# Kernel optimization log

Measured on AMD Instinct MI355X. Metric: run time of the kernel, lower is better.

Reference implementation:

```python
import jax, jax.numpy as jnp
import numpy as np

H = 8  # heads
EPS = 1e-5


def adaln(x, t, W, b):
    # AdaLayerNorm: emb = Linear(t); scale, shift = chunk(emb, 2, dim=-1)
    emb = t @ W + b                      # [B,1,2*D]
    scale, shift = jnp.split(emb, 2, axis=-1)
    mu = jnp.mean(x, axis=-1, keepdims=True)
    var = jnp.var(x, axis=-1, keepdims=True)
    xn = (x - mu) / jnp.sqrt(var + EPS)  # elementwise_affine=False
    return xn * (1.0 + scale) + shift


def attention(x, ctx, Wq, Wk, Wv, Wo, bo):
    B, N, D = x.shape
    d = D // H
    q = (x @ Wq).reshape(B, N, H, d).transpose(0, 2, 1, 3)          # [B,H,N,d]
    k = (ctx @ Wk).reshape(B, ctx.shape[1], H, d).transpose(0, 2, 1, 3)
    v = (ctx @ Wv).reshape(B, ctx.shape[1], H, d).transpose(0, 2, 1, 3)
    sim = jnp.einsum('bhid,bhjd->bhij', q, k) * (d ** -0.5)
    attn = jax.nn.softmax(sim, axis=-1)
    out = jnp.einsum('bhij,bhjd->bhid', attn, v)
    out = out.transpose(0, 2, 1, 3).reshape(B, N, D)
    return out @ Wo + bo


def geglu_ff(x, W1, b1, W2, b2):
    u, g = jnp.split(x @ W1 + b1, 2, axis=-1)
    return (u * jax.nn.gelu(g, approximate=False)) @ W2 + b2


def setup_inputs() -> dict:
    key = jax.random.key(0)
    ks = jax.random.split(key, 16)
    D = 512
    s = 0.02
    inp = {
        'x': jax.random.normal(ks[0], (2, 2048, D), jnp.float32),
        't': jax.random.normal(ks[1], (2, 1, D), jnp.float32),
        'cond': jax.random.normal(ks[2], (2, 1024, D), jnp.float32),
        'n1_w': jax.random.normal(ks[3], (D, 2 * D), jnp.float32) * s,
        'n1_b': jnp.zeros((2 * D,), jnp.float32),
        'n2_w': jax.random.normal(ks[4], (D, 2 * D), jnp.float32) * s,
        'n2_b': jnp.zeros((2 * D,), jnp.float32),
        'n4_w': jax.random.normal(ks[5], (D, 2 * D), jnp.float32) * s,
        'n4_b': jnp.zeros((2 * D,), jnp.float32),
        'a1_q': jax.random.normal(ks[6], (D, D), jnp.float32) * s,
        'a1_k': jax.random.normal(ks[7], (D, D), jnp.float32) * s,
        'a1_v': jax.random.normal(ks[8], (D, D), jnp.float32) * s,
        'a1_o': jax.random.normal(ks[9], (D, D), jnp.float32) * s,
        'a1_ob': jnp.zeros((D,), jnp.float32),
        'a2_q': jax.random.normal(ks[10], (D, D), jnp.float32) * s,
        'a2_k': jax.random.normal(ks[11], (D, D), jnp.float32) * s,
        'a2_v': jax.random.normal(ks[12], (D, D), jnp.float32) * s,
        'a2_o': jax.random.normal(ks[13], (D, D), jnp.float32) * s,
        'a2_ob': jnp.zeros((D,), jnp.float32),
        'ff_w1': jax.random.normal(ks[14], (D, 8 * D), jnp.float32) * s,
        'ff_b1': jnp.zeros((8 * D,), jnp.float32),
        'ff_w2': jax.random.normal(ks[15], (4 * D, D), jnp.float32) * s,
        'ff_b2': jnp.zeros((D,), jnp.float32),
    }
    return inp


def reference(x, t, cond, n1_w, n1_b, n2_w, n2_b, n4_w, n4_b,
              a1_q, a1_k, a1_v, a1_o, a1_ob,
              a2_q, a2_k, a2_v, a2_o, a2_ob,
              ff_w1, ff_b1, ff_w2, ff_b2):
    # BasicTransformerBlock, is_deform=False, withT=False, inference (dropout/droppath = identity, LayerScale = identity since init_values=0)
    h = adaln(x, t, n1_w, n1_b)
    x = attention(h, h, a1_q, a1_k, a1_v, a1_o, a1_ob) + x
    h = adaln(x, t, n2_w, n2_b)
    x = attention(h, cond, a2_q, a2_k, a2_v, a2_o, a2_ob) + x
    h = adaln(x, t, n4_w, n4_b)
    x = geglu_ff(h, ff_w1, ff_b1, ff_w2, ff_b2) + x
    return x
```

## Files before the change

kernel.cpp:

```cpp
#include <hip/hip_runtime.h>
#include <math.h>

#define D_MODEL 512
#define NHEADS  8
#define DHEAD   64

typedef __bf16  bf16x2 __attribute__((ext_vector_type(2)));
typedef __bf16  bf16x4 __attribute__((ext_vector_type(4)));
typedef __bf16  bf16x8 __attribute__((ext_vector_type(8)));
typedef float   f32x4  __attribute__((ext_vector_type(4)));

__global__ __launch_bounds__(256) void adaln_params_kernel(
        const float* __restrict__ t,
        const float* __restrict__ w1, const float* __restrict__ b1,
        const float* __restrict__ w2, const float* __restrict__ b2,
        const float* __restrict__ w4, const float* __restrict__ b4,
        float* __restrict__ emb, int B) {
    int g = blockIdx.x * blockDim.x + threadIdx.x;
    int per = B * 2 * D_MODEL;
    if (g >= 3 * per) return;
    int norm = g / per;
    int rem  = g - norm * per;
    int b = rem / (2 * D_MODEL);
    int c = rem % (2 * D_MODEL);
    const float* W  = (norm == 0) ? w1 : (norm == 1 ? w2 : w4);
    const float* bb = (norm == 0) ? b1 : (norm == 1 ? b2 : b4);
    const float* trow = t + (size_t)b * D_MODEL;
    float acc = bb[c];
    for (int k = 0; k < D_MODEL; ++k)
        acc = fmaf(trow[k], W[(size_t)k * (2 * D_MODEL) + c], acc);
    emb[g] = acc;
}

__global__ __launch_bounds__(256) void adaln_apply_kernel(
        const float* __restrict__ x, const float* __restrict__ emb_n,
        __bf16* __restrict__ h, int N) {
    int row = blockIdx.x;
    int b = row / N;
    const float* xr = x + (size_t)row * D_MODEL;
    int tid = threadIdx.x;
    float2 v = *(const float2*)(xr + 2 * tid);
    float s = v.x + v.y, sq = v.x * v.x + v.y * v.y;
#pragma unroll
    for (int off = 32; off; off >>= 1) {
        s  += __shfl_xor(s, off);
        sq += __shfl_xor(sq, off);
    }
    __shared__ float rs[4], rq[4];
    if ((tid & 63) == 0) { rs[tid >> 6] = s; rq[tid >> 6] = sq; }
    __syncthreads();
    float tot  = rs[0] + rs[1] + rs[2] + rs[3];
    float totq = rq[0] + rq[1] + rq[2] + rq[3];
    float mu  = tot * (1.0f / D_MODEL);
    float var = totq * (1.0f / D_MODEL) - mu * mu;
    float inv = rsqrtf(var + 1e-5f);
    const float* er = emb_n + (size_t)b * (2 * D_MODEL);
    float2 sc = *(const float2*)(er + 2 * tid);
    float2 sh = *(const float2*)(er + D_MODEL + 2 * tid);
    bf16x2 o;
    o[0] = (__bf16)((v.x - mu) * inv * (1.0f + sc.x) + sh.x);
    o[1] = (__bf16)((v.y - mu) * inv * (1.0f + sc.y) + sh.y);
    *(bf16x2*)(h + (size_t)row * D_MODEL + 2 * tid) = o;
}

__global__ __launch_bounds__(256) void convert_bf16v_kernel(
        const float* __restrict__ src, __bf16* __restrict__ dst, int n) {
    int i = (blockIdx.x * 256 + threadIdx.x) * 4;
    if (i >= n) return;
    float4 v = *(const float4*)(src + i);
    bf16x2 a, b;
    a[0] = (__bf16)v.x; a[1] = (__bf16)v.y;
    b[0] = (__bf16)v.z; b[1] = (__bf16)v.w;
    *(bf16x2*)(dst + i)     = a;
    *(bf16x2*)(dst + i + 2) = b;
}

__device__ __forceinline__ void transpose_tile(
        const float* __restrict__ src, __bf16* __restrict__ dst,
        int K, int N, int k0, int n0) {
    __shared__ float t[64][65];
    int tid = threadIdx.x;
    int r = tid >> 6, c = tid & 63;
#pragma unroll
    for (int i = 0; i < 16; ++i)
        t[r + 4 * i][c] = src[(size_t)(k0 + r + 4 * i) * N + n0 + c];
    __syncthreads();
#pragma unroll
    for (int i = 0; i < 16; ++i)
        dst[(size_t)(n0 + r + 4 * i) * K + k0 + c] = (__bf16)t[c][r + 4 * i];
}

struct WPtrs8 { const float* s[8]; __bf16* d[8]; };

__global__ __launch_bounds__(256) void convt8_kernel(WPtrs8 p) {
    int w = blockIdx.z;
    transpose_tile(p.s[w], p.d[w], 512, 512, blockIdx.y * 64, blockIdx.x * 64);
}

__global__ __launch_bounds__(256) void convt_kernel(
        const float* __restrict__ src, __bf16* __restrict__ dst, int K, int N) {
    transpose_tile(src, dst, K, N, blockIdx.y * 64, blockIdx.x * 64);
}

template<int OUT>
__global__ __launch_bounds__(256) void gemm_bf16_kernel(
        const __bf16* __restrict__ A, const __bf16* __restrict__ Bt,
        const float* __restrict__ bias, const float* __restrict__ res,
        void* __restrict__ Cv, int M, int K, int N) {
    __shared__ __attribute__((aligned(16))) __bf16 As[128][72];
    __shared__ __attribute__((aligned(16))) __bf16 Bs[64][72];
    int tid = threadIdx.x;
    int wave = tid >> 6, lane = tid & 63;
    int wr = wave >> 1, wc = wave & 1;
    int r = lane & 15, g = lane >> 4;
    int m0 = blockIdx.y << 7, n0 = blockIdx.x << 6;

    int sr = tid >> 3, sk = (tid & 7) << 3;
    const __bf16* Ap = A  + (size_t)(m0 + sr) * K + sk;
    const __bf16* Bp = Bt + (size_t)(n0 + sr) * K + sk;

    f32x4 acc[4][2];
#pragma unroll
    for (int mi = 0; mi < 4; ++mi)
#pragma unroll
        for (int ni = 0; ni < 2; ++ni) acc[mi][ni] = (f32x4){0.f, 0.f, 0.f, 0.f};

    for (int k0 = 0; k0 < K; k0 += 64) {
#pragma unroll
        for (int i = 0; i < 4; ++i)
            *(bf16x8*)&As[sr + 32 * i][sk] = *(const bf16x8*)(Ap + (size_t)(32 * i) * K + k0);
#pragma unroll
        for (int i = 0; i < 2; ++i)
            *(bf16x8*)&Bs[sr + 32 * i][sk] = *(const bf16x8*)(Bp + (size_t)(32 * i) * K + k0);
        __syncthreads();
#pragma unroll
        for (int kk = 0; kk < 2; ++kk) {
            bf16x8 af[4], bfr[2];
#pragma unroll
            for (int mi = 0; mi < 4; ++mi)
                af[mi] = *(const bf16x8*)&As[(wr << 6) + (mi << 4) + r][(kk << 5) + (g << 3)];
#pragma unroll
            for (int ni = 0; ni < 2; ++ni)
                bfr[ni] = *(const bf16x8*)&Bs[(wc << 5) + (ni << 4) + r][(kk << 5) + (g << 3)];
#pragma unroll
            for (int mi = 0; mi < 4; ++mi)
#pragma unroll
                for (int ni = 0; ni < 2; ++ni)
                    acc[mi][ni] = __builtin_amdgcn_mfma_f32_16x16x32_bf16(
                        af[mi], bfr[ni], acc[mi][ni], 0, 0, 0);
        }
        __syncthreads();
    }

#pragma unroll
    for (int mi = 0; mi < 4; ++mi) {
#pragma unroll
        for (int ni = 0; ni < 2; ++ni) {
            int col = n0 + (wc << 5) + (ni << 4) + r;
            float scl = (OUT == 2 && col < 512) ? 0.125f : 1.0f;
#pragma unroll
            for (int rg = 0; rg < 4; ++rg) {
                int row = m0 + (wr << 6) + (mi << 4) + (g << 2) + rg;
                if (OUT == 1) {
                    float v = acc[mi][ni][rg] + bias[col] + res[(size_t)row * N + col];
                    ((float*)Cv)[(size_t)row * N + col] = v;
                } else {
                    ((__bf16*)Cv)[(size_t)row * N + col] = (__bf16)(acc[mi][ni][rg] * scl);
                }
            }
        }
    }
}

__global__ __launch_bounds__(256) void gemm_geglu_bf16_kernel(
        const __bf16* __restrict__ A, const __bf16* __restrict__ W1t,
        const float* __restrict__ b1, __bf16* __restrict__ gg, int M, int K) {
    const int NOUT = 4 * D_MODEL;
    __shared__ __attribute__((aligned(16))) __bf16 As[128][72];
    __shared__ __attribute__((aligned(16))) __bf16 Bu[64][72];
    __shared__ __attribute__((aligned(16))) __bf16 Bg[64][72];
    int tid = threadIdx.x;
    int wave = tid >> 6, lane = tid & 63;
    int wr = wave >> 1, wc = wave & 1;
    int r = lane & 15, g = lane >> 4;
    int m0 = blockIdx.y << 7, n0 = blockIdx.x << 6;

    int sr = tid >> 3, sk = (tid & 7) << 3;
    const __bf16* Ap = A   + (size_t)(m0 + sr) * K + sk;
    const __bf16* Up = W1t + (size_t)(n0 + sr) * K + sk;
    const __bf16* Gp = W1t + (size_t)(NOUT + n0 + sr) * K + sk;

    f32x4 accu[4][2], accg[4][2];
#pragma unroll
    for (int mi = 0; mi < 4; ++mi)
#pragma unroll
        for (int ni = 0; ni < 2; ++ni) {
            accu[mi][ni] = (f32x4){0.f, 0.f, 0.f, 0.f};
            accg[mi][ni] = (f32x4){0.f, 0.f, 0.f, 0.f};
        }

    for (int k0 = 0; k0 < K; k0 += 64) {
#pragma unroll
        for (int i = 0; i < 4; ++i)
            *(bf16x8*)&As[sr + 32 * i][sk] = *(const bf16x8*)(Ap + (size_t)(32 * i) * K + k0);
#pragma unroll
        for (int i = 0; i < 2; ++i) {
            *(bf16x8*)&Bu[sr + 32 * i][sk] = *(const bf16x8*)(Up + (size_t)(32 * i) * K + k0);
            *(bf16x8*)&Bg[sr + 32 * i][sk] = *(const bf16x8*)(Gp + (size_t)(32 * i) * K + k0);
        }
        __syncthreads();
#pragma unroll
        for (int kk = 0; kk < 2; ++kk) {
            bf16x8 af[4], bu[2], bg[2];
#pragma unroll
            for (int mi = 0; mi < 4; ++mi)
                af[mi] = *(const bf16x8*)&As[(wr << 6) + (mi << 4) + r][(kk << 5) + (g << 3)];
#pragma unroll
            for (int ni = 0; ni < 2; ++ni) {
                bu[ni] = *(const bf16x8*)&Bu[(wc << 5) + (ni << 4) + r][(kk << 5) + (g << 3)];
                bg[ni] = *(const bf16x8*)&Bg[(wc << 5) + (ni << 4) + r][(kk << 5) + (g << 3)];
            }
#pragma unroll
            for (int mi = 0; mi < 4; ++mi)
#pragma unroll
                for (int ni = 0; ni < 2; ++ni) {
                    accu[mi][ni] = __builtin_amdgcn_mfma_f32_16x16x32_bf16(
                        af[mi], bu[ni], accu[mi][ni], 0, 0, 0);
                    accg[mi][ni] = __builtin_amdgcn_mfma_f32_16x16x32_bf16(
                        af[mi], bg[ni], accg[mi][ni], 0, 0, 0);
                }
        }
        __syncthreads();
    }

#pragma unroll
    for (int mi = 0; mi < 4; ++mi) {
#pragma unroll
        for (int ni = 0; ni < 2; ++ni) {
            int col = n0 + (wc << 5) + (ni << 4) + r;
            float bu_ = b1[col], bg_ = b1[NOUT + col];
#pragma unroll
            for (int rg = 0; rg < 4; ++rg) {
                int row = m0 + (wr << 6) + (mi << 4) + (g << 2) + rg;
                float u  = accu[mi][ni][rg] + bu_;
                float gv = accg[mi][ni][rg] + bg_;
                float ge = 0.5f * gv * (1.0f + erff(gv * 0.70710678118654752f));
                gg[(size_t)row * NOUT + col] = (__bf16)(u * ge);
            }
        }
    }
}

__global__ __launch_bounds__(256) void attn_mfma_kernel(
        const __bf16* __restrict__ q, const __bf16* __restrict__ k,
        const __bf16* __restrict__ v, __bf16* __restrict__ o,
        int Nq, int Nk, int sq, int skv) {
    __shared__ __attribute__((aligned(16))) __bf16 Ks[64][72];
    __shared__ __attribute__((aligned(16))) __bf16 Vt[64 * 72];
    __shared__ __attribute__((aligned(16))) __bf16 Pl[4][16][72];

    int tid = threadIdx.x;
    int w = tid >> 6, lane = tid & 63;
    int r = lane & 15, g = lane >> 4;

    int nqb = Nq >> 6;
    int qb = blockIdx.x % nqb;
    int hh = (blockIdx.x / nqb) % NHEADS;
    int b  = blockIdx.x / (nqb * NHEADS);

    const __bf16* qp = q + ((size_t)(b * Nq + (qb << 6) + (w << 4) + r)) * sq
                         + hh * DHEAD + (g << 3);
    bf16x8 qf0 = *(const bf16x8*)qp;
    bf16x8 qf1 = *(const bf16x8*)(qp + 32);

    int krow = tid >> 2, kcb = (tid & 3) << 4;
    int va = tid & 31,  vbb = tid >> 5;
    size_t kvbase = (size_t)b * Nk * skv + (size_t)hh * DHEAD;
    const __bf16* kp = k + kvbase + (size_t)krow * skv + kcb;
    const __bf16* vp = v + kvbase + (size_t)(2 * va) * skv + (vbb << 3);

    f32x4 oacc[4];
#pragma unroll
    for (int dt = 0; dt < 4; ++dt) oacc[dt] = (f32x4){0.f, 0.f, 0.f, 0.f};
    float m = -1e30f, l = 0.f;

    bf16x8 kr0 = *(const bf16x8*)kp;
    bf16x8 kr1 = *(const bf16x8*)(kp + 8);
    bf16x8 vr0 = *(const bf16x8*)vp;
    bf16x8 vr1 = *(const bf16x8*)(vp + skv);
    {
        *(bf16x8*)&Ks[krow][kcb]     = kr0;
        *(bf16x8*)&Ks[krow][kcb + 8] = kr1;
        int blk = (va >> 2) ^ vbb;
        int cw  = ((va & 3) << 1);
#pragma unroll
        for (int j = 0; j < 8; ++j) {
            bf16x2 pr; pr[0] = vr0[j]; pr[1] = vr1[j];
            *(bf16x2*)&Vt[(size_t)(8 * vbb + j) * 72 + blk * 8 + cw] = pr;
        }
    }
    __syncthreads();

    int ntiles = Nk >> 6;
    for (int t = 0; t < ntiles; ++t) {
        bool pre = (t + 1 < ntiles);
        if (pre) {
            const __bf16* kp2 = kp + (size_t)(t + 1) * 64 * skv;
            const __bf16* vp2 = vp + (size_t)(t + 1) * 64 * skv;
            kr0 = *(const bf16x8*)kp2;
            kr1 = *(const bf16x8*)(kp2 + 8);
            vr0 = *(const bf16x8*)vp2;
            vr1 = *(const bf16x8*)(vp2 + skv);
        }

        f32x4 sacc[4];
#pragma unroll
        for (int nt = 0; nt < 4; ++nt) sacc[nt] = (f32x4){0.f, 0.f, 0.f, 0.f};
        __builtin_amdgcn_s_setprio(1);
#pragma unroll
        for (int nt = 0; nt < 4; ++nt) {
            bf16x8 kf0 = *(const bf16x8*)&Ks[(nt << 4) + r][g << 3];
            bf16x8 kf1 = *(const bf16x8*)&Ks[(nt << 4) + r][32 + (g << 3)];
            sacc[nt] = __builtin_amdgcn_mfma_f32_16x16x32_bf16(kf0, qf0, sacc[nt], 0, 0, 0);
            sacc[nt] = __builtin_amdgcn_mfma_f32_16x16x32_bf16(kf1, qf1, sacc[nt], 0, 0, 0);
        }
        __builtin_amdgcn_s_setprio(0);

        float mx = sacc[0][0];
#pragma unroll
        for (int nt = 0; nt < 4; ++nt)
#pragma unroll
            for (int rg = 0; rg < 4; ++rg) mx = fmaxf(mx, sacc[nt][rg]);
        mx = fmaxf(mx, __shfl_xor(mx, 16));
        mx = fmaxf(mx, __shfl_xor(mx, 32));
        float mn = fmaxf(m, mx);
        float al = __expf(m - mn);
        m = mn;
        float sum = 0.f;
#pragma unroll
        for (int nt = 0; nt < 4; ++nt) {
            bf16x4 pk;
#pragma unroll
            for (int rg = 0; rg < 4; ++rg) {
                float p = __expf(sacc[nt][rg] - mn);
                sum += p;
                pk[rg] = (__bf16)p;
            }
            *(bf16x4*)&Pl[w][r][(nt << 4) + (g << 2)] = pk;
        }
        sum += __shfl_xor(sum, 16);
        sum += __shfl_xor(sum, 32);
        l = l * al + sum;
#pragma unroll
        for (int dt = 0; dt < 4; ++dt)
#pragma unroll
            for (int rg = 0; rg < 4; ++rg) oacc[dt][rg] *= al;

        __builtin_amdgcn_s_setprio(1);
#pragma unroll
        for (int kh = 0; kh < 2; ++kh) {
            bf16x8 pa = *(const bf16x8*)&Pl[w][r][(kh << 5) + (g << 3)];
#pragma unroll
            for (int dt = 0; dt < 4; ++dt) {
                int row = (dt << 4) + r;
                int blk = ((kh << 2) + g) ^ ((row >> 3) & 7);
                bf16x8 vf = *(const bf16x8*)&Vt[(size_t)row * 72 + (blk << 3)];
                oacc[dt] = __builtin_amdgcn_mfma_f32_16x16x32_bf16(vf, pa, oacc[dt], 0, 0, 0);
            }
        }
        __builtin_amdgcn_s_setprio(0);

        __syncthreads();
        if (pre) {
            *(bf16x8*)&Ks[krow][kcb]     = kr0;
            *(bf16x8*)&Ks[krow][kcb + 8] = kr1;
            int blk = (va >> 2) ^ vbb;
            int cw  = ((va & 3) << 1);
#pragma unroll
            for (int j = 0; j < 8; ++j) {
                bf16x2 pr; pr[0] = vr0[j]; pr[1] = vr1[j];
                *(bf16x2*)&Vt[(size_t)(8 * vbb + j) * 72 + blk * 8 + cw] = pr;
            }
        }
        __syncthreads();
    }

    float inv = 1.0f / l;
    __bf16* ob = o + ((size_t)(b * Nq + (qb << 6) + (w << 4) + r)) * D_MODEL + hh * DHEAD;
#pragma unroll
    for (int dt = 0; dt < 4; ++dt) {
        bf16x4 ov;
#pragma unroll
        for (int rg = 0; rg < 4; ++rg) ov[rg] = (__bf16)(oacc[dt][rg] * inv);
        *(bf16x4*)&ob[(dt << 4) + (g << 2)] = ov;
    }
}

extern "C" void kernel_launch(void* const* d_in, const int* in_sizes, int n_in,
                              void* d_out, int out_size, void* d_ws, size_t ws_size,
                              hipStream_t stream) {
    const float* x    = (const float*)d_in[0];
    const float* t    = (const float*)d_in[1];
    const float* cond = (const float*)d_in[2];
    const float* n1_w = (const float*)d_in[3];
    const float* n1_b = (const float*)d_in[4];
    const float* n2_w = (const float*)d_in[5];
    const float* n2_b = (const float*)d_in[6];
    const float* n4_w = (const float*)d_in[7];
    const float* n4_b = (const float*)d_in[8];
    const float* a1_q = (const float*)d_in[9];
    const float* a1_k = (const float*)d_in[10];
    const float* a1_v = (const float*)d_in[11];
    const float* a1_o = (const float*)d_in[12];
    const float* a1_ob= (const float*)d_in[13];
    const float* a2_q = (const float*)d_in[14];
    const float* a2_k = (const float*)d_in[15];
    const float* a2_v = (const float*)d_in[16];
    const float* a2_o = (const float*)d_in[17];
    const float* a2_ob= (const float*)d_in[18];
    const float* ff_w1= (const float*)d_in[19];
    const float* ff_b1= (const float*)d_in[20];
    const float* ff_w2= (const float*)d_in[21];
    const float* ff_b2= (const float*)d_in[22];
    float* out = (float*)d_out;

    const int B  = in_sizes[1] / D_MODEL;
    const int N  = in_sizes[0] / (B * D_MODEL);
    const int Nc = in_sizes[2] / (B * D_MODEL);
    const int R  = B * N;
    const int Rc = B * Nc;

    char* Wb = (char*)d_ws;
    float* emb   = (float*)Wb;
    __bf16* r1   = (__bf16*)(Wb + 32768);
    __bf16* qkv  = r1;
    __bf16* q2   = r1;
    __bf16* kv2  = r1 + (size_t)R * 512;
    __bf16* gg   = r1;
    __bf16* h_bf = (__bf16*)(Wb + 32768 + 16777216);
    __bf16* c_bf = (__bf16*)(Wb + 32768 + 16777216 + 4194304);
    __bf16* wts  = (__bf16*)(Wb + 32768 + 16777216 + 4194304 + 2097152);
    __bf16* a1_qt = wts;
    __bf16* a1_ot = wts + 3 * 262144;
    __bf16* a2_qt = wts + 4 * 262144;
    __bf16* a2_kt = wts + 5 * 262144;
    __bf16* a2_ot = wts + 7 * 262144;
    __bf16* ff1t  = wts + 8 * 262144;
    __bf16* ff2t  = ff1t + 2097152;

    dim3 blk(256);

    adaln_params_kernel<<<dim3((3 * B * 2 * D_MODEL + 255) / 256), blk, 0, stream>>>(
        t, n1_w, n1_b, n2_w, n2_b, n4_w, n4_b, emb, B);

    WPtrs8 wp;
    wp.s[0] = a1_q; wp.s[1] = a1_k; wp.s[2] = a1_v; wp.s[3] = a1_o;
    wp.s[4] = a2_q; wp.s[5] = a2_k; wp.s[6] = a2_v; wp.s[7] = a2_o;
    wp.d[0] = a1_qt; wp.d[1] = wts + 262144; wp.d[2] = wts + 2 * 262144; wp.d[3] = a1_ot;
    wp.d[4] = a2_qt; wp.d[5] = a2_kt; wp.d[6] = wts + 6 * 262144; wp.d[7] = a2_ot;
    convt8_kernel<<<dim3(8, 8, 8), blk, 0, stream>>>(wp);
    convt_kernel<<<dim3(64, 8), blk, 0, stream>>>(ff_w1, ff1t, 512, 4096);
    convt_kernel<<<dim3(8, 32), blk, 0, stream>>>(ff_w2, ff2t, 2048, 512);
    convert_bf16v_kernel<<<dim3(Rc * D_MODEL / 1024), blk, 0, stream>>>(
        cond, c_bf, Rc * D_MODEL);

    adaln_apply_kernel<<<dim3(R), blk, 0, stream>>>(x, emb, h_bf, N);
    gemm_bf16_kernel<2><<<dim3(24, R / 128), blk, 0, stream>>>(
        h_bf, a1_qt, nullptr, nullptr, qkv, R, 512, 1536);
    attn_mfma_kernel<<<dim3(B * NHEADS * (N / 64)), blk, 0, stream>>>(
        qkv, qkv + 512, qkv + 1024, h_bf, N, N, 1536, 1536);
    gemm_bf16_kernel<1><<<dim3(8, R / 128), blk, 0, stream>>>(
        h_bf, a1_ot, a1_ob, x, out, R, 512, 512);

    adaln_apply_kernel<<<dim3(R), blk, 0, stream>>>(
        out, emb + (size_t)B * 2 * D_MODEL, h_bf, N);
    gemm_bf16_kernel<0><<<dim3(16, Rc / 128), blk, 0, stream>>>(
        c_bf, a2_kt, nullptr, nullptr, kv2, Rc, 512, 1024);
    gemm_bf16_kernel<2><<<dim3(8, R / 128), blk, 0, stream>>>(
        h_bf, a2_qt, nullptr, nullptr, q2, R, 512, 512);
    attn_mfma_kernel<<<dim3(B * NHEADS * (N / 64)), blk, 0, stream>>>(
        q2, kv2, kv2 + 512, h_bf, N, Nc, 512, 1024);
    gemm_bf16_kernel<1><<<dim3(8, R / 128), blk, 0, stream>>>(
        h_bf, a2_ot, a2_ob, out, out, R, 512, 512);

    adaln_apply_kernel<<<dim3(R), blk, 0, stream>>>(
        out, emb + (size_t)2 * B * 2 * D_MODEL, h_bf, N);
    gemm_geglu_bf16_kernel<<<dim3(32, R / 128), blk, 0, stream>>>(
        h_bf, ff1t, ff_b1, gg, R, 512);
    gemm_bf16_kernel<1><<<dim3(8, R / 128), blk, 0, stream>>>(
        gg, ff2t, ff_b2, out, out, R, 2048, 512);
}
```

Baseline: 251.4 us.

## Use direct global-to-LDS loads with swizzle, fuse prep kernels, lazy softmax rescale

Several independent changes land together. The GEMM kernels now load tiles straight from global memory into LDS (global_load_lds) into an XOR-swizzled unpadded layout, drop one barrier per k-step, and gain a template for a smaller 64-row block that is used for the N=512 GEMMs to give more blocks. The four preprocessing kernels (adaln params, weight transposes, cond conversion) are merged into one launch. The attention kernel skips the online-softmax rescale when the running max grows by less than 8, and swizzles the P tile in LDS to reduce bank conflicts. Risks are synchronization hazards from the removed trailing barrier and numeric effects from the deferred max.

```diff
diff --git a/kernel.cpp b/kernel.cpp
--- a/kernel.cpp
+++ b/kernel.cpp
@@ -10,26 +10,73 @@
 typedef __bf16  bf16x8 __attribute__((ext_vector_type(8)));
 typedef float   f32x4  __attribute__((ext_vector_type(4)));
 
-__global__ __launch_bounds__(256) void adaln_params_kernel(
-        const float* __restrict__ t,
-        const float* __restrict__ w1, const float* __restrict__ b1,
-        const float* __restrict__ w2, const float* __restrict__ b2,
-        const float* __restrict__ w4, const float* __restrict__ b4,
-        float* __restrict__ emb, int B) {
-    int g = blockIdx.x * blockDim.x + threadIdx.x;
-    int per = B * 2 * D_MODEL;
-    if (g >= 3 * per) return;
-    int norm = g / per;
-    int rem  = g - norm * per;
-    int b = rem / (2 * D_MODEL);
-    int c = rem % (2 * D_MODEL);
-    const float* W  = (norm == 0) ? w1 : (norm == 1 ? w2 : w4);
-    const float* bb = (norm == 0) ? b1 : (norm == 1 ? b2 : b4);
-    const float* trow = t + (size_t)b * D_MODEL;
-    float acc = bb[c];
-    for (int k = 0; k < D_MODEL; ++k)
-        acc = fmaf(trow[k], W[(size_t)k * (2 * D_MODEL) + c], acc);
-    emb[g] = acc;
+__device__ __forceinline__ void gload16(const __bf16* g, __bf16* l) {
+    __builtin_amdgcn_global_load_lds(
+        (const __attribute__((address_space(1))) unsigned int*)g,
+        (__attribute__((address_space(3))) unsigned int*)l, 16, 0, 0);
+}
+
+__device__ __forceinline__ void transpose_tile(
+        const float* __restrict__ src, __bf16* __restrict__ dst,
+        int K, int N, int k0, int n0) {
+    __shared__ float t[64][65];
+    int tid = threadIdx.x;
+    int r = tid >> 6, c = tid & 63;
+#pragma unroll
+    for (int i = 0; i < 16; ++i)
+        t[r + 4 * i][c] = src[(size_t)(k0 + r + 4 * i) * N + n0 + c];
+    __syncthreads();
+#pragma unroll
+    for (int i = 0; i < 16; ++i)
+        dst[(size_t)(n0 + r + 4 * i) * K + k0 + c] = (__bf16)t[c][r + 4 * i];
+}
+
+struct PrepArgs {
+    const float *t, *n1w, *n1b, *n2w, *n2b, *n4w, *n4b;
+    float* emb;
+    const float* ws[8]; __bf16* wd[8];
+    const float *ffw1, *ffw2;
+    __bf16 *ff1t, *ff2t;
+    const float* cond; __bf16* cbf;
+    int B, condN;
+};
+
+__global__ __launch_bounds__(256) void prep_kernel(PrepArgs a) {
+    int bb = blockIdx.x, tid = threadIdx.x;
+    if (bb < 24) {
+        int gI = bb * 256 + tid;
+        int per = a.B * 2 * D_MODEL;
+        if (gI >= 3 * per) return;
+        int norm = gI / per;
+        int rem  = gI - norm * per;
+        int b = rem / (2 * D_MODEL);
+        int c = rem % (2 * D_MODEL);
+        const float* W  = (norm == 0) ? a.n1w : (norm == 1 ? a.n2w : a.n4w);
+        const float* bb_= (norm == 0) ? a.n1b : (norm == 1 ? a.n2b : a.n4b);
+        const float* trow = a.t + (size_t)b * D_MODEL;
+        float acc = bb_[c];
+        for (int k = 0; k < D_MODEL; ++k)
+            acc = fmaf(trow[k], W[(size_t)k * (2 * D_MODEL) + c], acc);
+        a.emb[gI] = acc;
+    } else if (bb < 536) {
+        int w = (bb - 24) >> 6, tI = (bb - 24) & 63;
+        transpose_tile(a.ws[w], a.wd[w], 512, 512, (tI >> 3) << 6, (tI & 7) << 6);
+    } else if (bb < 1048) {
+        int tI = bb - 536;
+        transpose_tile(a.ffw1, a.ff1t, 512, 4096, (tI & 7) << 6, (tI >> 3) << 6);
+    } else if (bb < 1304) {
+        int tI = bb - 1048;
+        transpose_tile(a.ffw2, a.ff2t, 2048, 512, (tI >> 3) << 6, (tI & 7) << 6);
+    } else {
+        int i = ((bb - 1304) * 256 + tid) * 4;
+        if (i >= a.condN) return;
+        float4 v = *(const float4*)(a.cond + i);
+        bf16x2 p0, p1;
+        p0[0] = (__bf16)v.x; p0[1] = (__bf16)v.y;
+        p1[0] = (__bf16)v.z; p1[1] = (__bf16)v.w;
+        *(bf16x2*)(a.cbf + i)     = p0;
+        *(bf16x2*)(a.cbf + i + 2) = p1;
+    }
 }
 
 __global__ __launch_bounds__(256) void adaln_apply_kernel(
@@ -63,104 +110,72 @@
     *(bf16x2*)(h + (size_t)row * D_MODEL + 2 * tid) = o;
 }
 
-__global__ __launch_bounds__(256) void convert_bf16v_kernel(
-        const float* __restrict__ src, __bf16* __restrict__ dst, int n) {
-    int i = (blockIdx.x * 256 + threadIdx.x) * 4;
-    if (i >= n) return;
-    float4 v = *(const float4*)(src + i);
-    bf16x2 a, b;
-    a[0] = (__bf16)v.x; a[1] = (__bf16)v.y;
-    b[0] = (__bf16)v.z; b[1] = (__bf16)v.w;
-    *(bf16x2*)(dst + i)     = a;
-    *(bf16x2*)(dst + i + 2) = b;
-}
-
-__device__ __forceinline__ void transpose_tile(
-        const float* __restrict__ src, __bf16* __restrict__ dst,
-        int K, int N, int k0, int n0) {
-    __shared__ float t[64][65];
-    int tid = threadIdx.x;
-    int r = tid >> 6, c = tid & 63;
-#pragma unroll
-    for (int i = 0; i < 16; ++i)
-        t[r + 4 * i][c] = src[(size_t)(k0 + r + 4 * i) * N + n0 + c];
-    __syncthreads();
-#pragma unroll
-    for (int i = 0; i < 16; ++i)
-        dst[(size_t)(n0 + r + 4 * i) * K + k0 + c] = (__bf16)t[c][r + 4 * i];
-}
-
-struct WPtrs8 { const float* s[8]; __bf16* d[8]; };
-
-__global__ __launch_bounds__(256) void convt8_kernel(WPtrs8 p) {
-    int w = blockIdx.z;
-    transpose_tile(p.s[w], p.d[w], 512, 512, blockIdx.y * 64, blockIdx.x * 64);
-}
-
-__global__ __launch_bounds__(256) void convt_kernel(
-        const float* __restrict__ src, __bf16* __restrict__ dst, int K, int N) {
-    transpose_tile(src, dst, K, N, blockIdx.y * 64, blockIdx.x * 64);
-}
-
-template<int OUT>
+template<int OUT, int WM>
 __global__ __launch_bounds__(256) void gemm_bf16_kernel(
         const __bf16* __restrict__ A, const __bf16* __restrict__ Bt,
         const float* __restrict__ bias, const float* __restrict__ res,
         void* __restrict__ Cv, int M, int K, int N) {
-    __shared__ __attribute__((aligned(16))) __bf16 As[128][72];
-    __shared__ __attribute__((aligned(16))) __bf16 Bs[64][72];
+    constexpr int BM = 2 * WM;
+    constexpr int MI = WM / 16;
+    __shared__ __attribute__((aligned(16))) __bf16 As[BM * 64];
+    __shared__ __attribute__((aligned(16))) __bf16 Bs[64 * 64];
     int tid = threadIdx.x;
     int wave = tid >> 6, lane = tid & 63;
     int wr = wave >> 1, wc = wave & 1;
     int r = lane & 15, g = lane >> 4;
-    int m0 = blockIdx.y << 7, n0 = blockIdx.x << 6;
-
-    int sr = tid >> 3, sk = (tid & 7) << 3;
-    const __bf16* Ap = A  + (size_t)(m0 + sr) * K + sk;
-    const __bf16* Bp = Bt + (size_t)(n0 + sr) * K + sk;
-
-    f32x4 acc[4][2];
-#pragma unroll
-    for (int mi = 0; mi < 4; ++mi)
+    int rx = r & 7;
+    int m0 = blockIdx.y * BM, n0 = blockIdx.x << 6;
+
+    int lrow = lane >> 3;
+    int lcol = ((lane & 7) ^ lrow) << 3;
+    const __bf16* Ag = A  + (size_t)(m0 + (wave << 3) + lrow) * K + lcol;
+    const __bf16* Bg = Bt + (size_t)(n0 + (wave << 3) + lrow) * K + lcol;
+    __bf16* AsW = As + (size_t)(wave << 3) * 64;
+    __bf16* BsW = Bs + (size_t)(wave << 3) * 64;
+
+    f32x4 acc[MI][2];
+#pragma unroll
+    for (int mi = 0; mi < MI; ++mi)
 #pragma unroll
         for (int ni = 0; ni < 2; ++ni) acc[mi][ni] = (f32x4){0.f, 0.f, 0.f, 0.f};
 
     for (int k0 = 0; k0 < K; k0 += 64) {
-#pragma unroll
-        for (int i = 0; i < 4; ++i)
-            *(bf16x8*)&As[sr + 32 * i][sk] = *(const bf16x8*)(Ap + (size_t)(32 * i) * K + k0);
-#pragma unroll
-        for (int i = 0; i < 2; ++i)
-            *(bf16x8*)&Bs[sr + 32 * i][sk] = *(const bf16x8*)(Bp + (size_t)(32 * i) * K + k0);
+        if (k0) __syncthreads();
+#pragma unroll
+        for (int i = 0; i < MI; ++i)
+            gload16(Ag + (size_t)(i * 32) * K + k0, AsW + i * 32 * 64);
+#pragma unroll
+        for (int j = 0; j < 2; ++j)
+            gload16(Bg + (size_t)(j * 32) * K + k0, BsW + j * 32 * 64);
         __syncthreads();
 #pragma unroll
         for (int kk = 0; kk < 2; ++kk) {
-            bf16x8 af[4], bfr[2];
-#pragma unroll
-            for (int mi = 0; mi < 4; ++mi)
-                af[mi] = *(const bf16x8*)&As[(wr << 6) + (mi << 4) + r][(kk << 5) + (g << 3)];
+            int cs = ((((kk << 2) + g) ^ rx) << 3);
+            bf16x8 af[MI], bf_[2];
+#pragma unroll
+            for (int mi = 0; mi < MI; ++mi)
+                af[mi] = *(const bf16x8*)&As[(size_t)(wr * WM + (mi << 4) + r) * 64 + cs];
 #pragma unroll
             for (int ni = 0; ni < 2; ++ni)
-                bfr[ni] = *(const bf16x8*)&Bs[(wc << 5) + (ni << 4) + r][(kk << 5) + (g << 3)];
-#pragma unroll
-            for (int mi = 0; mi < 4; ++mi)
+                bf_[ni] = *(const bf16x8*)&Bs[(size_t)((wc << 5) + (ni << 4) + r) * 64 + cs];
+#pragma unroll
+            for (int mi = 0; mi < MI; ++mi)
 #pragma unroll
                 for (int ni = 0; ni < 2; ++ni)
                     acc[mi][ni] = __builtin_amdgcn_mfma_f32_16x16x32_bf16(
-                        af[mi], bfr[ni], acc[mi][ni], 0, 0, 0);
-        }
-        __syncthreads();
-    }
-
-#pragma unroll
-    for (int mi = 0; mi < 4; ++mi) {
+                        af[mi], bf_[ni], acc[mi][ni], 0, 0, 0);
+        }
+    }
+
+#pragma unroll
+    for (int mi = 0; mi < MI; ++mi) {
 #pragma unroll
         for (int ni = 0; ni < 2; ++ni) {
             int col = n0 + (wc << 5) + (ni << 4) + r;
             float scl = (OUT == 2 && col < 512) ? 0.125f : 1.0f;
 #pragma unroll
             for (int rg = 0; rg < 4; ++rg) {
-                int row = m0 + (wr << 6) + (mi << 4) + (g << 2) + rg;
+                int row = m0 + wr * WM + (mi << 4) + (g << 2) + rg;
                 if (OUT == 1) {
                     float v = acc[mi][ni][rg] + bias[col] + res[(size_t)row * N + col];
                     ((float*)Cv)[(size_t)row * N + col] = v;
@@ -176,19 +191,24 @@
         const __bf16* __restrict__ A, const __bf16* __restrict__ W1t,
         const float* __restrict__ b1, __bf16* __restrict__ gg, int M, int K) {
     const int NOUT = 4 * D_MODEL;
-    __shared__ __attribute__((aligned(16))) __bf16 As[128][72];
-    __shared__ __attribute__((aligned(16))) __bf16 Bu[64][72];
-    __shared__ __attribute__((aligned(16))) __bf16 Bg[64][72];
+    __shared__ __attribute__((aligned(16))) __bf16 AsL[128 * 64];
+    __shared__ __attribute__((aligned(16))) __bf16 BuL[64 * 64];
+    __shared__ __attribute__((aligned(16))) __bf16 BgL[64 * 64];
     int tid = threadIdx.x;
     int wave = tid >> 6, lane = tid & 63;
     int wr = wave >> 1, wc = wave & 1;
     int r = lane & 15, g = lane >> 4;
+    int rx = r & 7;
     int m0 = blockIdx.y << 7, n0 = blockIdx.x << 6;
 
-    int sr = tid >> 3, sk = (tid & 7) << 3;
-    const __bf16* Ap = A   + (size_t)(m0 + sr) * K + sk;
-    const __bf16* Up = W1t + (size_t)(n0 + sr) * K + sk;
-    const __bf16* Gp = W1t + (size_t)(NOUT + n0 + sr) * K + sk;
+    int lrow = lane >> 3;
+    int lcol = ((lane & 7) ^ lrow) << 3;
+    const __bf16* Ag = A   + (size_t)(m0 + (wave << 3) + lrow) * K + lcol;
+    const __bf16* Ug = W1t + (size_t)(n0 + (wave << 3) + lrow) * K + lcol;
+    const __bf16* Gg = W1t + (size_t)(NOUT + n0 + (wave << 3) + lrow) * K + lcol;
+    __bf16* AsW = AsL + (size_t)(wave << 3) * 64;
+    __bf16* BuW = BuL + (size_t)(wave << 3) * 64;
+    __bf16* BgW = BgL + (size_t)(wave << 3) * 64;
 
     f32x4 accu[4][2], accg[4][2];
 #pragma unroll
@@ -200,25 +220,27 @@
         }
 
     for (int k0 = 0; k0 < K; k0 += 64) {
+        if (k0) __syncthreads();
 #pragma unroll
         for (int i = 0; i < 4; ++i)
-            *(bf16x8*)&As[sr + 32 * i][sk] = *(const bf16x8*)(Ap + (size_t)(32 * i) * K + k0);
-#pragma unroll
-        for (int i = 0; i < 2; ++i) {
-            *(bf16x8*)&Bu[sr + 32 * i][sk] = *(const bf16x8*)(Up + (size_t)(32 * i) * K + k0);
-            *(bf16x8*)&Bg[sr + 32 * i][sk] = *(const bf16x8*)(Gp + (size_t)(32 * i) * K + k0);
+            gload16(Ag + (size_t)(i * 32) * K + k0, AsW + i * 32 * 64);
+#pragma unroll
+        for (int j = 0; j < 2; ++j) {
+            gload16(Ug + (size_t)(j * 32) * K + k0, BuW + j * 32 * 64);
+            gload16(Gg + (size_t)(j * 32) * K + k0, BgW + j * 32 * 64);
         }
         __syncthreads();
 #pragma unroll
         for (int kk = 0; kk < 2; ++kk) {
+            int cs = ((((kk << 2) + g) ^ rx) << 3);
             bf16x8 af[4], bu[2], bg[2];
 #pragma unroll
             for (int mi = 0; mi < 4; ++mi)
-                af[mi] = *(const bf16x8*)&As[(wr << 6) + (mi << 4) + r][(kk << 5) + (g << 3)];
+                af[mi] = *(const bf16x8*)&AsL[(size_t)((wr << 6) + (mi << 4) + r) * 64 + cs];
 #pragma unroll
             for (int ni = 0; ni < 2; ++ni) {
-                bu[ni] = *(const bf16x8*)&Bu[(wc << 5) + (ni << 4) + r][(kk << 5) + (g << 3)];
-                bg[ni] = *(const bf16x8*)&Bg[(wc << 5) + (ni << 4) + r][(kk << 5) + (g << 3)];
+                bu[ni] = *(const bf16x8*)&BuL[(size_t)((wc << 5) + (ni << 4) + r) * 64 + cs];
+                bg[ni] = *(const bf16x8*)&BgL[(size_t)((wc << 5) + (ni << 4) + r) * 64 + cs];
             }
 #pragma unroll
             for (int mi = 0; mi < 4; ++mi)
@@ -230,7 +252,6 @@
                         af[mi], bg[ni], accg[mi][ni], 0, 0, 0);
                 }
         }
-        __syncthreads();
     }
 
 #pragma unroll
@@ -333,9 +354,17 @@
             for (int rg = 0; rg < 4; ++rg) mx = fmaxf(mx, sacc[nt][rg]);
         mx = fmaxf(mx, __shfl_xor(mx, 16));
         mx = fmaxf(mx, __shfl_xor(mx, 32));
-        float mn = fmaxf(m, mx);
-        float al = __expf(m - mn);
-        m = mn;
+        bool defer = __all(mx <= m + 8.0f);
+        float mn = defer ? m : fmaxf(m, mx);
+        if (!defer) {
+            float al = __expf(m - mn);
+            m = mn;
+            l *= al;
+#pragma unroll
+            for (int dt = 0; dt < 4; ++dt)
+#pragma unroll
+                for (int rg = 0; rg < 4; ++rg) oacc[dt][rg] *= al;
+        }
         float sum = 0.f;
 #pragma unroll
         for (int nt = 0; nt < 4; ++nt) {
@@ -346,20 +375,17 @@
                 sum += p;
                 pk[rg] = (__bf16)p;
             }
-            *(bf16x4*)&Pl[w][r][(nt << 4) + (g << 2)] = pk;
+            *(bf16x4*)&Pl[w][r][((nt ^ (r & 3)) << 4) + (g << 2)] = pk;
         }
         sum += __shfl_xor(sum, 16);
         sum += __shfl_xor(sum, 32);
-        l = l * al + sum;
-#pragma unroll
-        for (int dt = 0; dt < 4; ++dt)
-#pragma unroll
-            for (int rg = 0; rg < 4; ++rg) oacc[dt][rg] *= al;
+        l += sum;
 
         __builtin_amdgcn_s_setprio(1);
 #pragma unroll
         for (int kh = 0; kh < 2; ++kh) {
-            bf16x8 pa = *(const bf16x8*)&Pl[w][r][(kh << 5) + (g << 3)];
+            int bb_ = (kh << 1) + (g >> 1);
+            bf16x8 pa = *(const bf16x8*)&Pl[w][r][((bb_ ^ (r & 3)) << 4) + ((g & 1) << 3)];
 #pragma unroll
             for (int dt = 0; dt < 4; ++dt) {
                 int row = (dt << 4) + r;
@@ -450,43 +476,40 @@
 
     dim3 blk(256);
 
-    adaln_params_kernel<<<dim3((3 * B * 2 * D_MODEL + 255) / 256), blk, 0, stream>>>(
-        t, n1_w, n1_b, n2_w, n2_b, n4_w, n4_b, emb, B);
-
-    WPtrs8 wp;
-    wp.s[0] = a1_q; wp.s[1] = a1_k; wp.s[2] = a1_v; wp.s[3] = a1_o;
-    wp.s[4] = a2_q; wp.s[5] = a2_k; wp.s[6] = a2_v; wp.s[7] = a2_o;
-    wp.d[0] = a1_qt; wp.d[1] = wts + 262144; wp.d[2] = wts + 2 * 262144; wp.d[3] = a1_ot;
-    wp.d[4] = a2_qt; wp.d[5] = a2_kt; wp.d[6] = wts + 6 * 262144; wp.d[7] = a2_ot;
-    convt8_kernel<<<dim3(8, 8, 8), blk, 0, stream>>>(wp);
-    convt_kernel<<<dim3(64, 8), blk, 0, stream>>>(ff_w1, ff1t, 512, 4096);
-    convt_kernel<<<dim3(8, 32), blk, 0, stream>>>(ff_w2, ff2t, 2048, 512);
-    convert_bf16v_kernel<<<dim3(Rc * D_MODEL / 1024), blk, 0, stream>>>(
-        cond, c_bf, Rc * D_MODEL);
+    PrepArgs pa;
+    pa.t = t; pa.n1w = n1_w; pa.n1b = n1_b; pa.n2w = n2_w; pa.n2b = n2_b;
+    pa.n4w = n4_w; pa.n4b = n4_b; pa.emb = emb;
+    pa.ws[0] = a1_q; pa.ws[1] = a1_k; pa.ws[2] = a1_v; pa.ws[3] = a1_o;
+    pa.ws[4] = a2_q; pa.ws[5] = a2_k; pa.ws[6] = a2_v; pa.ws[7] = a2_o;
+    pa.wd[0] = a1_qt; pa.wd[1] = wts + 262144; pa.wd[2] = wts + 2 * 262144; pa.wd[3] = a1_ot;
+    pa.wd[4] = a2_qt; pa.wd[5] = a2_kt; pa.wd[6] = wts + 6 * 262144; pa.wd[7] = a2_ot;
+    pa.ffw1 = ff_w1; pa.ffw2 = ff_w2; pa.ff1t = ff1t; pa.ff2t = ff2t;
+    pa.cond = cond; pa.cbf = c_bf; pa.B = B; pa.condN = Rc * D_MODEL;
+    prep_kernel<<<dim3(1304 + (Rc * D_MODEL) / 1024), blk, 0, stream>>>(pa);
 
     adaln_apply_kernel<<<dim3(R), blk, 0, stream>>>(x, emb, h_bf, N);
-    gemm_bf16_kernel<2><<<dim3(24, R / 128), blk, 0, stream>>>(
+    gemm_bf16_kernel<2, 64><<<dim3(24, R / 128), blk, 0, stream>>>(
         h_bf, a1_qt, nullptr, nullptr, qkv, R, 512, 1536);
     attn_mfma_kernel<<<dim3(B * NHEADS * (N / 64)), blk, 0, stream>>>(
         qkv, qkv + 512, qkv + 1024, h_bf, N, N, 1536, 1536);
-    gemm_bf16_kernel<1><<<dim3(8, R / 128), blk, 0, stream>>>(
+    gemm_bf16_kernel<1, 32><<<dim3(8, R / 64), blk, 0, stream>>>(
         h_bf, a1_ot, a1_ob, x, out, R, 512, 512);
 
     adaln_apply_kernel<<<dim3(R), blk, 0, stream>>>(
         out, emb + (size_t)B * 2 * D_MODEL, h_bf, N);
-    gemm_bf16_kernel<0><<<dim3(16, Rc / 128), blk, 0, stream>>>(
+    gemm_bf16_kernel<0, 32><<<dim3(16, Rc / 64), blk, 0, stream>>>(
         c_bf, a2_kt, nullptr, nullptr, kv2, Rc, 512, 1024);
-    gemm_bf16_kernel<2><<<dim3(8, R / 128), blk, 0, stream>>>(
+    gemm_bf16_kernel<2, 32><<<dim3(8, R / 64), blk, 0, stream>>>(
         h_bf, a2_qt, nullptr, nullptr, q2, R, 512, 512);
     attn_mfma_kernel<<<dim3(B * NHEADS * (N / 64)), blk, 0, stream>>>(
         q2, kv2, kv2 + 512, h_bf, N, Nc, 512, 1024);
-    gemm_bf16_kernel<1><<<dim3(8, R / 128), blk, 0, stream>>>(
+    gemm_bf16_kernel<1, 32><<<dim3(8, R / 64), blk, 0, stream>>>(
         h_bf, a2_ot, a2_ob, out, out, R, 512, 512);
 
     adaln_apply_kernel<<<dim3(R), blk, 0, stream>>>(
         out, emb + (size_t)2 * B * 2 * D_MODEL, h_bf, N);
     gemm_geglu_bf16_kernel<<<dim3(32, R / 128), blk, 0, stream>>>(
         h_bf, ff1t, ff_b1, gg, R, 512);
-    gemm_bf16_kernel<1><<<dim3(8, R / 128), blk, 0, stream>>>(
+    gemm_bf16_kernel<1, 32><<<dim3(8, R / 64), blk, 0, stream>>>(
         gg, ff2t, ff_b2, out, out, R, 2048, 512);
 }
```

Result: faster. 229.5 us (-8.7%).
